# Kernel optimization log

Hardware: AMD Instinct MI355X
Metric: run time of the kernel (lower is better)

The kernel has to match this reference:

```python
import jax, jax.numpy as jnp
import numpy as np

B, S, D, H = 4, 2048, 512, 8
KD = D // H          # key_dim == head_dim == 64
FFN = 4 * D

def _ln(x, g, b, eps):
    mu = x.mean(-1, keepdims=True)
    var = ((x - mu) ** 2).mean(-1, keepdims=True)
    return (x - mu) / jnp.sqrt(var + eps) * g + b

def setup_inputs():
    key = jax.random.key(0)
    ks = jax.random.split(key, 8)
    def lin(k, o, i, scale=0.02):
        k1, k2 = jax.random.split(k)
        return (jax.random.normal(k1, (o, i), jnp.float32) * scale,
                jax.random.normal(k2, (o,), jnp.float32) * scale)
    wq, bq = lin(ks[0], D, D)
    wk, bk = lin(ks[1], D, D)
    wv, bv = lin(ks[2], D, D)
    wg, bg = lin(ks[3], D, D)
    wo, bo = lin(ks[4], D, D)
    fc1_w, fc1_b = lin(ks[5], FFN, D)
    fc2_w, fc2_b = lin(ks[6], D, FFN)
    return {
        'src': jax.random.normal(ks[7], (B, S, D), jnp.float32),
        'mask': jnp.zeros((S, S), jnp.bool_),
        'padding_mask': jnp.zeros((B, S), jnp.bool_),
        'wq': wq, 'bq': bq, 'wk': wk, 'bk': bk, 'wv': wv, 'bv': bv,
        'wg': wg, 'bg': bg, 'wo': wo, 'bo': bo,
        'fc1_w': fc1_w, 'fc1_b': fc1_b, 'fc2_w': fc2_w, 'fc2_b': fc2_b,
        'ln_ffn_g': jnp.ones((FFN,), jnp.float32), 'ln_ffn_b': jnp.zeros((FFN,), jnp.float32),
        'n0_g': jnp.ones((D,), jnp.float32), 'n0_b': jnp.zeros((D,), jnp.float32),
        'n1_g': jnp.ones((D,), jnp.float32), 'n1_b': jnp.zeros((D,), jnp.float32),
    }

def reference(src, mask, padding_mask, wq, bq, wk, bk, wv, bv, wg, bg, wo, bo,
              fc1_w, fc1_b, fc2_w, fc2_b, ln_ffn_g, ln_ffn_b, n0_g, n0_b, n1_g, n1_b):
    b, s, d = src.shape
    # RetNet per-head decay mask (h, s, s): exp((i-j)*log(gamma_h)) on the lower triangle,
    # row-normalized by sqrt(row sum) (torchscale RetNetRelPos, parallel mode).
    idx = jnp.arange(s)
    diff = (idx[:, None] - idx[None, :]).astype(src.dtype)
    decay = jnp.log(1.0 - 2.0 ** (-5.0 - jnp.arange(H, dtype=src.dtype)))
    dm = jnp.where(diff[None] >= 0, jnp.exp(diff[None] * decay[:, None, None]), 0.0)
    dm = dm / jnp.sqrt(dm.sum(-1, keepdims=True))
    # projections; k scaled by key_dim**-0.5 before head split
    q = (src @ wq.T + bq).reshape(b, s, H, KD).transpose(0, 2, 1, 3)
    k = ((src @ wk.T + bk) * (KD ** -0.5)).reshape(b, s, H, KD).transpose(0, 2, 1, 3)
    v = src @ wv.T + bv
    g = src @ wg.T + bg
    # parallel retention: additive decay bias, detached L1 row normalization
    qk = jnp.einsum('bhid,bhjd->bhij', q, k) + dm[None]
    den = jnp.maximum(jnp.abs(jax.lax.stop_gradient(qk).sum(-1, keepdims=True)), 1.0)
    qk = qk / den
    vr = v.reshape(b, s, H, KD).transpose(0, 2, 1, 3)
    o = jnp.einsum('bhij,bhjd->bhid', qk, vr).transpose(0, 2, 1, 3)  # (b,s,h,hd)
    # per-head LayerNorm, eps=1e-6, no affine
    mu = o.mean(-1, keepdims=True)
    o = (o - mu) / jnp.sqrt(((o - mu) ** 2).mean(-1, keepdims=True) + 1e-6)
    o = jax.nn.silu(g) * o.reshape(b, s, d)
    o = o @ wo.T + bo
    # post-norm residual layout
    x = _ln(src + o, n0_g, n0_b, 1e-5)
    h = jax.nn.gelu(x @ fc1_w.T + fc1_b, approximate=False)
    h = _ln(h, ln_ffn_g, ln_ffn_b, 1e-6)  # subln
    h = h @ fc2_w.T + fc2_b
    return _ln(x + h, n1_g, n1_b, 1e-5)
```

## Files before the change

### kernel.cpp

```cpp
#include <hip/hip_runtime.h>
#include <hip/hip_bf16.h>
#include <math.h>

#define DEV __device__ __forceinline__

typedef __attribute__((ext_vector_type(4))) float f32x4;
typedef __attribute__((ext_vector_type(16))) float f32x16;
typedef __attribute__((ext_vector_type(8))) short bf16x8;
typedef __attribute__((ext_vector_type(8))) unsigned short u16x8;
typedef unsigned short u16;
typedef unsigned int u32;
typedef __attribute__((ext_vector_type(4))) u32 u32x4;

DEV u16 f2bf(float f) {
  union { float f; u32 u; } v; v.f = f;
  u32 r = v.u + 0x7fffu + ((v.u >> 16) & 1u);
  return (u16)(r >> 16);
}
DEV float bf2f(u16 h) {
  union { u32 u; float f; } v; v.u = ((u32)h) << 16;
  return v.f;
}

DEV void gl_lds16(const u16* g, u16* s) {
  __builtin_amdgcn_global_load_lds((const __attribute__((address_space(1))) void*)g,
                                   (__attribute__((address_space(3))) void*)s, 16, 0, 0);
}

DEV u32 cvt_pk_bf16(float lo, float hi) {
  u32 r;
  asm("v_cvt_pk_bf16_f32 %0, %1, %2" : "=v"(r) : "v"(lo), "v"(hi));
  return r;
}

DEV bf16x8 u4_to_bf8(u32x4 x) {
  union { u32x4 a; bf16x8 b; } u; u.a = x; return u.b;
}

#define MFMA16(a, b, c) __builtin_amdgcn_mfma_f32_16x16x32_bf16((a), (b), (c), 0, 0, 0)
#define MFMA32(a, b, c) __builtin_amdgcn_mfma_f32_32x32x16_bf16((a), (b), (c), 0, 0, 0)

DEV void cast8(const float* in, u16* out, float s) {
  f32x4 a = *(const f32x4*)in;
  f32x4 b = *(const f32x4*)(in + 4);
  u16x8 r;
  r[0] = f2bf(a[0] * s); r[1] = f2bf(a[1] * s); r[2] = f2bf(a[2] * s); r[3] = f2bf(a[3] * s);
  r[4] = f2bf(b[0] * s); r[5] = f2bf(b[1] * s); r[6] = f2bf(b[2] * s); r[7] = f2bf(b[3] * s);
  *(u16x8*)out = r;
}

__global__ __launch_bounds__(256) void prep_cast(
    const float* __restrict__ src, const float* __restrict__ wq, const float* __restrict__ wk,
    const float* __restrict__ wv, const float* __restrict__ wg, const float* __restrict__ wo,
    const float* __restrict__ fc1, const float* __restrict__ fc2,
    const float* __restrict__ bq, const float* __restrict__ bk,
    const float* __restrict__ bv, const float* __restrict__ bg,
    u16* __restrict__ src_bf, u16* __restrict__ Wcat, u16* __restrict__ wo_bf,
    u16* __restrict__ fc1_bf, u16* __restrict__ fc2_bf, float* __restrict__ bcat) {
  int u = blockIdx.x * 256 + threadIdx.x;
  if (u < 524288) {
    cast8(src + (size_t)u * 8, src_bf + (size_t)u * 8, 1.0f);
  } else if (u < 557056) {
    int v = u - 524288; cast8(wq + (size_t)v * 8, Wcat + (size_t)v * 8, 1.0f);
  } else if (u < 589824) {
    int v = u - 557056; cast8(wk + (size_t)v * 8, Wcat + 262144 + (size_t)v * 8, 0.125f);
  } else if (u < 622592) {
    int v = u - 589824; cast8(wv + (size_t)v * 8, Wcat + 524288 + (size_t)v * 8, 1.0f);
  } else if (u < 655360) {
    int v = u - 622592; cast8(wg + (size_t)v * 8, Wcat + 786432 + (size_t)v * 8, 1.0f);
  } else if (u < 688128) {
    int v = u - 655360; cast8(wo + (size_t)v * 8, wo_bf + (size_t)v * 8, 1.0f);
  } else if (u < 819200) {
    int v = u - 688128; cast8(fc1 + (size_t)v * 8, fc1_bf + (size_t)v * 8, 1.0f);
  } else if (u < 950272) {
    int v = u - 819200; cast8(fc2 + (size_t)v * 8, fc2_bf + (size_t)v * 8, 1.0f);
  } else if (u < 950528) {
    int v = u - 950272;
    #pragma unroll
    for (int e = 0; e < 8; e++) {
      int c = v * 8 + e;
      float val;
      if (c < 512)       val = bq[c];
      else if (c < 1024) val = bk[c - 512] * 0.125f;
      else if (c < 1536) val = bv[c - 1024];
      else               val = bg[c - 1536];
      bcat[c] = val;
    }
  }
}

template <int ACT>
__global__ __launch_bounds__(256) void gemm_v3(
    const u16* __restrict__ A, const u16* __restrict__ W, const float* __restrict__ bias,
    u16* __restrict__ Ob, int N, int K, int TN) {
  __shared__ __align__(16) u16 sm[2][16384];
  const int t = threadIdx.x, l = t & 63;
  const int w = t >> 6, wr = (w >> 1) * 64, wc = (w & 1) * 64;
  const int lc = l & 15, lch = l >> 4;
  const int NT = K >> 6;

  const int orig = blockIdx.x;
  const int cpx = gridDim.x >> 3;
  const int sid = (orig & 7) * cpx + (orig >> 3);
  const int bm = (sid / TN) * 128, bn = (sid % TN) * 128;

  const int srow = t >> 3, sc8 = t & 7;
  const u16* stA = A + (size_t)(bm + srow) * K + ((sc8 ^ (srow & 7)) * 8);
  const u16* stB = W + (size_t)(bn + srow) * K + ((sc8 ^ (srow & 7)) * 8);

#define STAGE(bidx, kt)                                                        \
  {                                                                            \
    u16* d = (u16*)sm[bidx] + t * 8;                                           \
    _Pragma("unroll")                                                          \
    for (int j = 0; j < 4; j++)                                                \
      gl_lds16(stA + (size_t)j * 32 * K + (kt), d + j * 2048);                 \
    _Pragma("unroll")                                                          \
    for (int j = 0; j < 4; j++)                                                \
      gl_lds16(stB + (size_t)j * 32 * K + (kt), d + 8192 + j * 2048);          \
  }

  f32x4 acc[4][4] = {};

  STAGE(0, 0)
  __syncthreads();

  for (int tt = 0; tt < NT; ++tt) {
    if (tt + 1 < NT) STAGE((tt + 1) & 1, (tt + 1) * 64)
    const u16* bufp = sm[tt & 1];
    bf16x8 af[4][2], bfv[4][2];
    #pragma unroll
    for (int mi = 0; mi < 4; mi++) {
      const int row = wr + mi * 16 + lc;
      #pragma unroll
      for (int ks = 0; ks < 2; ks++) {
        const int ch = ks * 4 + lch;
        af[mi][ks] = *(const bf16x8*)&bufp[row * 64 + ((ch ^ (row & 7)) * 8)];
      }
    }
    #pragma unroll
    for (int ni = 0; ni < 4; ni++) {
      const int row = wc + ni * 16 + lc;
      #pragma unroll
      for (int ks = 0; ks < 2; ks++) {
        const int ch = ks * 4 + lch;
        bfv[ni][ks] = *(const bf16x8*)&bufp[8192 + row * 64 + ((ch ^ (row & 7)) * 8)];
      }
    }
    #pragma unroll
    for (int ks = 0; ks < 2; ks++)
      #pragma unroll
      for (int mi = 0; mi < 4; mi++)
        #pragma unroll
        for (int ni = 0; ni < 4; ni++)
          acc[mi][ni] = MFMA16(af[mi][ks], bfv[ni][ks], acc[mi][ni]);
    __syncthreads();
  }
#undef STAGE

  u16* osm = (u16*)sm;
  #pragma unroll
  for (int ni = 0; ni < 4; ni++) {
    const int col = wc + ni * 16 + lc;
    const float bb = bias[bn + col];
    const int ckey = col >> 3, clow = col & 7;
    #pragma unroll
    for (int mi = 0; mi < 4; mi++) {
      #pragma unroll
      for (int r = 0; r < 4; r++) {
        const int row = wr + mi * 16 + lch * 4 + r;
        float v = acc[mi][ni][r] + bb;
        if (ACT == 1) v = 0.5f * v * (1.0f + erff(v * 0.70710678118f));
        osm[row * 128 + ((ckey ^ ((row & 7) << 1)) << 3) + clow] = f2bf(v);
      }
    }
  }
  __syncthreads();
  #pragma unroll
  for (int p = 0; p < 8; p++) {
    const int flat = p * 256 + t;
    const int row = flat >> 4, c = flat & 15;
    u16x8 y = *(const u16x8*)&osm[row * 128 + ((c ^ ((row & 7) << 1)) << 3)];
    *(u16x8*)&Ob[(size_t)(bm + row) * N + bn + c * 8] = y;
  }
}

template <int ACT>
__global__ __launch_bounds__(256) void gemm_m64(
    const u16* __restrict__ A, const u16* __restrict__ W, const float* __restrict__ bias,
    u16* __restrict__ Ob, int N, int K, int TN) {
  __shared__ __align__(16) u16 sm[2][12288];
  const int t = threadIdx.x, l = t & 63;
  const int w = t >> 6, wr = (w >> 1) * 32, wc = (w & 1) * 64;
  const int lc = l & 15, lch = l >> 4;
  const int NT = K >> 6;

  const int orig = blockIdx.x;
  const int cpx = gridDim.x >> 3;
  const int sid = (orig & 7) * cpx + (orig >> 3);
  const int bm = (sid / TN) * 64, bn = (sid % TN) * 128;

  const int srow = t >> 3, sc8 = t & 7;
  const u16* stA = A + (size_t)(bm + srow) * K + ((sc8 ^ (srow & 7)) * 8);
  const u16* stB = W + (size_t)(bn + srow) * K + ((sc8 ^ (srow & 7)) * 8);

#define STAGE(bidx, kt)                                                        \
  {                                                                            \
    u16* d = (u16*)sm[bidx] + t * 8;                                           \
    _Pragma("unroll")                                                          \
    for (int j = 0; j < 2; j++)                                                \
      gl_lds16(stA + (size_t)j * 32 * K + (kt), d + j * 2048);                 \
    _Pragma("unroll")                                                          \
    for (int j = 0; j < 4; j++)                                                \
      gl_lds16(stB + (size_t)j * 32 * K + (kt), d + 4096 + j * 2048);          \
  }

  f32x4 acc[2][4] = {};

  STAGE(0, 0)
  __syncthreads();

  for (int tt = 0; tt < NT; ++tt) {
    if (tt + 1 < NT) STAGE((tt + 1) & 1, (tt + 1) * 64)
    const u16* bufp = sm[tt & 1];
    bf16x8 af[2][2], bfv[4][2];
    #pragma unroll
    for (int mi = 0; mi < 2; mi++) {
      const int row = wr + mi * 16 + lc;
      #pragma unroll
      for (int ks = 0; ks < 2; ks++) {
        const int ch = ks * 4 + lch;
        af[mi][ks] = *(const bf16x8*)&bufp[row * 64 + ((ch ^ (row & 7)) * 8)];
      }
    }
    #pragma unroll
    for (int ni = 0; ni < 4; ni++) {
      const int row = wc + ni * 16 + lc;
      #pragma unroll
      for (int ks = 0; ks < 2; ks++) {
        const int ch = ks * 4 + lch;
        bfv[ni][ks] = *(const bf16x8*)&bufp[4096 + row * 64 + ((ch ^ (row & 7)) * 8)];
      }
    }
    #pragma unroll
    for (int ks = 0; ks < 2; ks++)
      #pragma unroll
      for (int mi = 0; mi < 2; mi++)
        #pragma unroll
        for (int ni = 0; ni < 4; ni++)
          acc[mi][ni] = MFMA16(af[mi][ks], bfv[ni][ks], acc[mi][ni]);
    __syncthreads();
  }
#undef STAGE

  u16* osm = (u16*)sm;
  #pragma unroll
  for (int ni = 0; ni < 4; ni++) {
    const int col = wc + ni * 16 + lc;
    const float bb = bias[bn + col];
    const int ckey = col >> 3, clow = col & 7;
    #pragma unroll
    for (int mi = 0; mi < 2; mi++) {
      #pragma unroll
      for (int r = 0; r < 4; r++) {
        const int row = wr + mi * 16 + lch * 4 + r;
        float v = acc[mi][ni][r] + bb;
        if (ACT == 1) v = 0.5f * v * (1.0f + erff(v * 0.70710678118f));
        osm[row * 128 + ((ckey ^ ((row & 7) << 1)) << 3) + clow] = f2bf(v);
      }
    }
  }
  __syncthreads();
  #pragma unroll
  for (int p = 0; p < 4; p++) {
    const int flat = p * 256 + t;
    const int row = flat >> 4, c = flat & 15;
    u16x8 y = *(const u16x8*)&osm[row * 128 + ((c ^ ((row & 7) << 1)) << 3)];
    *(u16x8*)&Ob[(size_t)(bm + row) * N + bn + c * 8] = y;
  }
}

__global__ __launch_bounds__(256) void vtrans(
    const u16* __restrict__ qkvg, u16* __restrict__ vtg) {
  __shared__ u16 L[64 * 72];
  const int t = threadIdx.x;
  const int jt = blockIdx.x * 64, bh = blockIdx.y, b = bh >> 3, h = bh & 7;
  const u16* src = qkvg + (size_t)(b * 2048 + jt) * 2048 + 1024 + h * 64;
  const int r0 = t >> 3, c0 = (t & 7) * 8;
  u16x8 a0 = *(const u16x8*)(src + (size_t)r0 * 2048 + c0);
  u16x8 a1 = *(const u16x8*)(src + (size_t)(r0 + 32) * 2048 + c0);
  #pragma unroll
  for (int e = 0; e < 8; e++) {
    L[(c0 + e) * 72 + r0] = a0[e];
    L[(c0 + e) * 72 + 32 + r0] = a1[e];
  }
  __syncthreads();
  u16* dst = vtg + (size_t)bh * 64 * 2048 + jt;
  *(u16x8*)(dst + (size_t)r0 * 2048 + c0) = *(const u16x8*)&L[r0 * 72 + c0];
  *(u16x8*)(dst + (size_t)(r0 + 32) * 2048 + c0) = *(const u16x8*)&L[(r0 + 32) * 72 + c0];
}

__global__ __launch_bounds__(512, 4) void retention_v3(
    const u16* __restrict__ qkvg, const u16* __restrict__ vtg, u16* __restrict__ gated) {
  const int S = 2048, DD = 2048;
  const int bh = blockIdx.x, b = bh >> 3, h = bh & 7;
  const int t = threadIdx.x, l = t & 63, w = t >> 6;
  const int lid = l & 31, hi = l >> 5;
  const int g = w >> 2, w4 = w & 3;
  const int wrow = blockIdx.y * 128 + w4 * 32;
  const int i_q = wrow + lid;

  __shared__ __align__(16) u16 sm[32768];

  const size_t base = (size_t)b * S * DD + (size_t)h * 64;
  const u16* qp = qkvg + base;
  const u16* kp = qkvg + base + 512;
  const u16* gp = qkvg + base + 1536;
  const u16* vtp = vtg + (size_t)bh * 64 * S;

  const float l2g = log2f(1.0f - exp2f(-5.0f - (float)h));
  const float rrs = rsqrtf((1.0f - exp2f((float)(i_q + 1) * l2g)) * exp2f(5.0f + (float)h));
  float bjc[16];
  #pragma unroll
  for (int r = 0; r < 16; r++) {
    int joff = (r & 3) + 8 * (r >> 2) + 4 * hi;
    bjc[r] = exp2f(-(float)joff * l2g);
  }

  bf16x8 qf[4];
  #pragma unroll
  for (int ks = 0; ks < 4; ks++)
    qf[ks] = *(const bf16x8*)(qp + (size_t)i_q * DD + ks * 16 + 8 * hi);

  f32x16 accO0, accO1;
  #pragma unroll
  for (int r = 0; r < 16; r++) { accO0[r] = 0.0f; accO1[r] = 0.0f; }
  float den_acc = 0.0f;

  const int srow = t >> 3, sc = t & 7;
  const u16* kg = kp + (size_t)srow * DD + ((sc ^ (srow & 7)) * 8);
  const u16* vg = vtp + (size_t)srow * S + ((sc ^ (srow & 7)) * 8);

#define RSTG(tile)                                                   \
  {                                                                  \
    const int sl_ = (tile) & 3;                                      \
    gl_lds16(kg + (size_t)(tile) * 64 * DD, sm + sl_ * 4096 + t * 8);\
    gl_lds16(vg + (tile) * 64, sm + 16384 + sl_ * 4096 + t * 8);     \
  }

  RSTG(0)
  RSTG(1)
  __syncthreads();

  for (int m = 0; m < 16; ++m) {
    if (m < 15) { RSTG(2 * m + 2) RSTG(2 * m + 3) }
    const int tile = 2 * m + g;
    const int jt = tile * 64;
    const u16* KsB = sm + (tile & 3) * 4096;
    const u16* VtB = sm + 16384 + (tile & 3) * 4096;

    #pragma unroll
    for (int jsub = 0; jsub < 2; jsub++) {
      f32x16 s;
      #pragma unroll
      for (int r = 0; r < 16; r++) s[r] = 0.0f;
      #pragma unroll
      for (int ks = 0; ks < 4; ks++) {
        bf16x8 kf = *(const bf16x8*)&KsB[(jsub * 32 + lid) * 64 +
                                         (((2 * ks + hi) ^ (lid & 7)) * 8)];
        s = MFMA32(kf, qf[ks], s);
      }
      {
        const int js = jt + jsub * 32;
        if (js <= wrow + 31) {
          float bcoef = exp2f((float)(i_q - js) * l2g) * rrs;
          if (js + 31 <= wrow) {
            #pragma unroll
            for (int r = 0; r < 16; r++) s[r] += bcoef * bjc[r];
          } else {
            const int dmax = i_q - js;
            #pragma unroll
            for (int r = 0; r < 16; r++) {
              int joff = (r & 3) + 8 * (r >> 2) + 4 * hi;
              s[r] += (joff <= dmax) ? bcoef * bjc[r] : 0.0f;
            }
          }
        }
      }
      #pragma unroll
      for (int r = 0; r < 16; r++) den_acc += s[r];
      u32 pk[8];
      #pragma unroll
      for (int q = 0; q < 4; q++) {
        pk[q * 2 + 0] = cvt_pk_bf16(s[4 * q + 0], s[4 * q + 1]);
        pk[q * 2 + 1] = cvt_pk_bf16(s[4 * q + 2], s[4 * q + 3]);
      }
      #pragma unroll
      for (int p = 0; p < 2; p++) {
        u32 own0 = hi ? pk[(2 * p + 1) * 2 + 0] : pk[(2 * p) * 2 + 0];
        u32 own1 = hi ? pk[(2 * p + 1) * 2 + 1] : pk[(2 * p) * 2 + 1];
        u32 snd0 = hi ? pk[(2 * p) * 2 + 0] : pk[(2 * p + 1) * 2 + 0];
        u32 snd1 = hi ? pk[(2 * p) * 2 + 1] : pk[(2 * p + 1) * 2 + 1];
        u32 r0 = __shfl_xor(snd0, 32);
        u32 r1 = __shfl_xor(snd1, 32);
        u32x4 paw;
        paw[0] = hi ? r0 : own0;
        paw[1] = hi ? r1 : own1;
        paw[2] = hi ? own0 : r0;
        paw[3] = hi ? own1 : r1;
        bf16x8 paf = u4_to_bf8(paw);
        const int jsl = jsub * 2 + p;
        bf16x8 vt0 = *(const bf16x8*)&VtB[lid * 64 + (((2 * jsl + hi) ^ (lid & 7)) * 8)];
        bf16x8 vt1 = *(const bf16x8*)&VtB[(32 + lid) * 64 + (((2 * jsl + hi) ^ (lid & 7)) * 8)];
        accO0 = MFMA32(vt0, paf, accO0);
        accO1 = MFMA32(vt1, paf, accO1);
      }
    }
    __syncthreads();
  }
#undef RSTG

  float* red = (float*)sm;
  const int ridx = (w4 * 64 + l) * 33;
  if (w >= 4) {
    #pragma unroll
    for (int r = 0; r < 16; r++) { red[ridx + r] = accO0[r]; red[ridx + 16 + r] = accO1[r]; }
    red[ridx + 32] = den_acc;
  }
  __syncthreads();
  if (w >= 4) return;
  #pragma unroll
  for (int r = 0; r < 16; r++) { accO0[r] += red[ridx + r]; accO1[r] += red[ridx + 16 + r]; }
  den_acc += red[ridx + 32];

  float den = den_acc + __shfl_xor(den_acc, 32);
  float rden = 1.0f / fmaxf(fabsf(den), 1.0f);
  float o0[16], o1[16];
  float s1 = 0.0f, s2 = 0.0f;
  #pragma unroll
  for (int r = 0; r < 16; r++) {
    o0[r] = accO0[r] * rden; s1 += o0[r]; s2 += o0[r] * o0[r];
    o1[r] = accO1[r] * rden; s1 += o1[r]; s2 += o1[r] * o1[r];
  }
  s1 += __shfl_xor(s1, 32);
  s2 += __shfl_xor(s2, 32);
  float mu = s1 * (1.0f / 64.0f);
  float var = s2 * (1.0f / 64.0f) - mu * mu;
  float rv = rsqrtf(var + 1e-6f);

  u16* Ot = sm + 16896 + w4 * 2304;
  #pragma unroll
  for (int r = 0; r < 16; r++) {
    int d = (r & 3) + 8 * (r >> 2) + 4 * hi;
    Ot[lid * 72 + d]      = f2bf((o0[r] - mu) * rv);
    Ot[lid * 72 + 32 + d] = f2bf((o1[r] - mu) * rv);
  }
  {
    const int i2 = l >> 1, half = l & 1;
    const int row = wrow + i2;
    #pragma unroll
    for (int c = 0; c < 4; c++) {
      u16x8 y8 = *(const u16x8*)&Ot[i2 * 72 + half * 32 + c * 8];
      u16x8 g8 = *(const u16x8*)(gp + (size_t)row * DD + half * 32 + c * 8);
      u16x8 o8;
      #pragma unroll
      for (int e = 0; e < 8; e++) {
        float gv = bf2f(g8[e]);
        float sg = gv / (1.0f + __expf(-gv));
        o8[e] = f2bf(bf2f(y8[e]) * sg);
      }
      *(u16x8*)&gated[((size_t)(b * S + row)) * 512 + h * 64 + half * 32 + c * 8] = o8;
    }
  }
}

__global__ __launch_bounds__(256) void add_ln512(
    const float* __restrict__ A, const u16* __restrict__ Bv,
    const float* __restrict__ gam, const float* __restrict__ bet, float eps,
    float* __restrict__ Of, u16* __restrict__ Ob) {
  int row = blockIdx.x * 4 + (threadIdx.x >> 6);
  int l = threadIdx.x & 63;
  const float* a = A + (size_t)row * 512 + l * 8;
  f32x4 a0 = *(const f32x4*)a, a1 = *(const f32x4*)(a + 4);
  u16x8 cv = *(const u16x8*)(Bv + (size_t)row * 512 + l * 8);
  float x[8];
  #pragma unroll
  for (int e = 0; e < 4; e++) { x[e] = a0[e] + bf2f(cv[e]); x[4 + e] = a1[e] + bf2f(cv[4 + e]); }
  float s = 0.f, s2 = 0.f;
  #pragma unroll
  for (int e = 0; e < 8; e++) { s += x[e]; s2 += x[e] * x[e]; }
  #pragma unroll
  for (int m = 1; m <= 32; m <<= 1) { s += __shfl_xor(s, m); s2 += __shfl_xor(s2, m); }
  float mu = s * (1.0f / 512.0f);
  float var = s2 * (1.0f / 512.0f) - mu * mu;
  float rinv = rsqrtf(var + eps);
  f32x4 g0 = *(const f32x4*)(gam + l * 8), g1 = *(const f32x4*)(gam + l * 8 + 4);
  f32x4 b0 = *(const f32x4*)(bet + l * 8), b1 = *(const f32x4*)(bet + l * 8 + 4);
  f32x4 y0, y1;
  #pragma unroll
  for (int e = 0; e < 4; e++) {
    y0[e] = (x[e] - mu) * rinv * g0[e] + b0[e];
    y1[e] = (x[4 + e] - mu) * rinv * g1[e] + b1[e];
  }
  float* op = Of + (size_t)row * 512 + l * 8;
  *(f32x4*)op = y0;
  *(f32x4*)(op + 4) = y1;
  if (Ob) {
    u16x8 rb_;
    #pragma unroll
    for (int e = 0; e < 4; e++) { rb_[e] = f2bf(y0[e]); rb_[4 + e] = f2bf(y1[e]); }
    *(u16x8*)(Ob + (size_t)row * 512 + l * 8) = rb_;
  }
}

__global__ __launch_bounds__(256) void subln_ffn(
    u16* __restrict__ hbuf, const float* __restrict__ gam, const float* __restrict__ bet) {
  int row = blockIdx.x * 4 + (threadIdx.x >> 6);
  int l = threadIdx.x & 63;
  u16* p = hbuf + (size_t)row * 2048;
  float x[32];
  #pragma unroll
  for (int cch = 0; cch < 4; cch++) {
    u16x8 v = *(const u16x8*)(p + cch * 512 + l * 8);
    #pragma unroll
    for (int e = 0; e < 8; e++) x[cch * 8 + e] = bf2f(v[e]);
  }
  float s = 0.f, s2 = 0.f;
  #pragma unroll
  for (int e = 0; e < 32; e++) { s += x[e]; s2 += x[e] * x[e]; }
  #pragma unroll
  for (int m = 1; m <= 32; m <<= 1) { s += __shfl_xor(s, m); s2 += __shfl_xor(s2, m); }
  float mu = s * (1.0f / 2048.0f);
  float var = s2 * (1.0f / 2048.0f) - mu * mu;
  float rinv = rsqrtf(var + 1e-6f);
  #pragma unroll
  for (int cch = 0; cch < 4; cch++) {
    int col = cch * 512 + l * 8;
    f32x4 g0 = *(const f32x4*)(gam + col), g1 = *(const f32x4*)(gam + col + 4);
    f32x4 b0 = *(const f32x4*)(bet + col), b1 = *(const f32x4*)(bet + col + 4);
    u16x8 o;
    #pragma unroll
    for (int e = 0; e < 4; e++) {
      o[e]     = f2bf((x[cch * 8 + e]     - mu) * rinv * g0[e] + b0[e]);
      o[4 + e] = f2bf((x[cch * 8 + 4 + e] - mu) * rinv * g1[e] + b1[e]);
    }
    *(u16x8*)(p + col) = o;
  }
}

extern "C" void kernel_launch(void* const* d_in, const int* in_sizes, int n_in,
                              void* d_out, int out_size, void* d_ws, size_t ws_size,
                              hipStream_t stream) {
  const float* src  = (const float*)d_in[0];
  const float* wq   = (const float*)d_in[3];
  const float* bq   = (const float*)d_in[4];
  const float* wk   = (const float*)d_in[5];
  const float* bk   = (const float*)d_in[6];
  const float* wv   = (const float*)d_in[7];
  const float* bv   = (const float*)d_in[8];
  const float* wg   = (const float*)d_in[9];
  const float* bg   = (const float*)d_in[10];
  const float* wo   = (const float*)d_in[11];
  const float* bo   = (const float*)d_in[12];
  const float* fc1w = (const float*)d_in[13];
  const float* fc1b = (const float*)d_in[14];
  const float* fc2w = (const float*)d_in[15];
  const float* fc2b = (const float*)d_in[16];
  const float* lng  = (const float*)d_in[17];
  const float* lnb  = (const float*)d_in[18];
  const float* n0g  = (const float*)d_in[19];
  const float* n0b  = (const float*)d_in[20];
  const float* n1g  = (const float*)d_in[21];
  const float* n1b  = (const float*)d_in[22];

  if (ws_size < 90710016u) return;

  char* ws = (char*)d_ws;
  u16*   src_bf = (u16*)(ws + 0);
  u16*   Wcat   = (u16*)(ws + 8388608);
  u16*   wo_bf  = (u16*)(ws + 10485760);
  u16*   fc1_bf = (u16*)(ws + 11010048);
  u16*   fc2_bf = (u16*)(ws + 13107200);
  float* bcat   = (float*)(ws + 15204352);
  u16*   qkvg   = (u16*)(ws + 15212544);
  u16*   gated  = (u16*)(ws + 48766976);
  u16*   attn   = (u16*)(ws + 57155584);
  float* xf     = (float*)(ws + 65544192);
  u16*   xbf    = (u16*)(ws + 82321408);
  u16*   vtg    = (u16*)(ws + 65544192);

  prep_cast<<<3713, 256, 0, stream>>>(src, wq, wk, wv, wg, wo, fc1w, fc2w,
                                      bq, bk, bv, bg,
                                      src_bf, Wcat, wo_bf, fc1_bf, fc2_bf, bcat);
  gemm_v3<0><<<1024, 256, 0, stream>>>(src_bf, Wcat, bcat, qkvg, 2048, 512, 16);
  vtrans<<<dim3(32, 32), 256, 0, stream>>>(qkvg, vtg);
  retention_v3<<<dim3(32, 16), 512, 0, stream>>>(qkvg, vtg, gated);
  gemm_m64<0><<<512, 256, 0, stream>>>(gated, wo_bf, bo, attn, 512, 512, 4);
  add_ln512<<<2048, 256, 0, stream>>>(src, attn, n0g, n0b, 1e-5f, xf, xbf);
  gemm_v3<1><<<1024, 256, 0, stream>>>(xbf, fc1_bf, fc1b, qkvg, 2048, 512, 16);
  subln_ffn<<<2048, 256, 0, stream>>>(qkvg, lng, lnb);
  gemm_m64<0><<<512, 256, 0, stream>>>(qkvg, fc2_bf, fc2b, attn, 512, 2048, 4);
  add_ln512<<<2048, 256, 0, stream>>>(xf, attn, n1g, n1b, 1e-5f, (float*)d_out, nullptr);
}
```

Baseline: 205.2 us.

## Give each retention wave its own query rows instead of splitting keys across wave groups

The retention kernel now assigns all 8 waves distinct 32-row query blocks (256 rows per workgroup) and has every wave stream all 32 key tiles, instead of two wave groups each covering half the key tiles and then reducing through LDS. Key and value staging becomes a double buffer with explicit vmcnt waits and raw barriers, and s_setprio is raised around the MFMA sections. This removes the cross-group LDS reduction and halves the LDS footprint. In exchange the grid is halved to 256 workgroups, so fewer workgroups are available to fill the CUs.

Measured after the change: 188.3 us. -8.2%, faster.

```diff
diff --git a/kernel.cpp b/kernel.cpp
--- a/kernel.cpp
+++ b/kernel.cpp
@@ -35,6 +35,14 @@
 
 DEV bf16x8 u4_to_bf8(u32x4 x) {
   union { u32x4 a; bf16x8 b; } u; u.a = x; return u.b;
+}
+
+DEV void barrier_() {
+  __builtin_amdgcn_sched_barrier(0);
+  asm volatile("" ::: "memory");
+  __builtin_amdgcn_s_barrier();
+  asm volatile("" ::: "memory");
+  __builtin_amdgcn_sched_barrier(0);
 }
 
 #define MFMA16(a, b, c) __builtin_amdgcn_mfma_f32_16x16x32_bf16((a), (b), (c), 0, 0, 0)
@@ -299,17 +307,16 @@
   *(u16x8*)(dst + (size_t)(r0 + 32) * 2048 + c0) = *(const u16x8*)&L[(r0 + 32) * 72 + c0];
 }
 
-__global__ __launch_bounds__(512, 4) void retention_v3(
+__global__ __launch_bounds__(512) void retention_v4(
     const u16* __restrict__ qkvg, const u16* __restrict__ vtg, u16* __restrict__ gated) {
   const int S = 2048, DD = 2048;
   const int bh = blockIdx.x, b = bh >> 3, h = bh & 7;
   const int t = threadIdx.x, l = t & 63, w = t >> 6;
   const int lid = l & 31, hi = l >> 5;
-  const int g = w >> 2, w4 = w & 3;
-  const int wrow = blockIdx.y * 128 + w4 * 32;
+  const int wrow = blockIdx.y * 256 + w * 32;
   const int i_q = wrow + lid;
 
-  __shared__ __align__(16) u16 sm[32768];
+  __shared__ __align__(16) u16 sm[18432];
 
   const size_t base = (size_t)b * S * DD + (size_t)h * 64;
   const u16* qp = qkvg + base;
@@ -340,35 +347,41 @@
   const u16* kg = kp + (size_t)srow * DD + ((sc ^ (srow & 7)) * 8);
   const u16* vg = vtp + (size_t)srow * S + ((sc ^ (srow & 7)) * 8);
 
-#define RSTG(tile)                                                   \
-  {                                                                  \
-    const int sl_ = (tile) & 3;                                      \
-    gl_lds16(kg + (size_t)(tile) * 64 * DD, sm + sl_ * 4096 + t * 8);\
-    gl_lds16(vg + (tile) * 64, sm + 16384 + sl_ * 4096 + t * 8);     \
+#define RSTG(tile)                                                    \
+  {                                                                   \
+    const int sl_ = (tile) & 1;                                       \
+    gl_lds16(kg + (size_t)(tile) * 64 * DD, sm + sl_ * 4096 + t * 8); \
+    gl_lds16(vg + (tile) * 64, sm + 8192 + sl_ * 4096 + t * 8);       \
   }
 
   RSTG(0)
-  RSTG(1)
-  __syncthreads();
-
-  for (int m = 0; m < 16; ++m) {
-    if (m < 15) { RSTG(2 * m + 2) RSTG(2 * m + 3) }
-    const int tile = 2 * m + g;
-    const int jt = tile * 64;
-    const u16* KsB = sm + (tile & 3) * 4096;
-    const u16* VtB = sm + 16384 + (tile & 3) * 4096;
+
+  for (int m = 0; m < 32; ++m) {
+    if (m < 31) {
+      RSTG(m + 1)
+      asm volatile("s_waitcnt vmcnt(2)" ::: "memory");
+    } else {
+      asm volatile("s_waitcnt vmcnt(0)" ::: "memory");
+    }
+    barrier_();
+
+    const int jt = m * 64;
+    const u16* KsB = sm + (m & 1) * 4096;
+    const u16* VtB = sm + 8192 + (m & 1) * 4096;
 
     #pragma unroll
     for (int jsub = 0; jsub < 2; jsub++) {
       f32x16 s;
       #pragma unroll
       for (int r = 0; r < 16; r++) s[r] = 0.0f;
+      __builtin_amdgcn_s_setprio(1);
       #pragma unroll
       for (int ks = 0; ks < 4; ks++) {
         bf16x8 kf = *(const bf16x8*)&KsB[(jsub * 32 + lid) * 64 +
                                          (((2 * ks + hi) ^ (lid & 7)) * 8)];
         s = MFMA32(kf, qf[ks], s);
       }
+      __builtin_amdgcn_s_setprio(0);
       {
         const int js = jt + jsub * 32;
         if (js <= wrow + 31) {
@@ -411,26 +424,16 @@
         const int jsl = jsub * 2 + p;
         bf16x8 vt0 = *(const bf16x8*)&VtB[lid * 64 + (((2 * jsl + hi) ^ (lid & 7)) * 8)];
         bf16x8 vt1 = *(const bf16x8*)&VtB[(32 + lid) * 64 + (((2 * jsl + hi) ^ (lid & 7)) * 8)];
+        __builtin_amdgcn_s_setprio(1);
         accO0 = MFMA32(vt0, paf, accO0);
         accO1 = MFMA32(vt1, paf, accO1);
-      }
-    }
-    __syncthreads();
+        __builtin_amdgcn_s_setprio(0);
+      }
+    }
+    asm volatile("s_waitcnt lgkmcnt(0)" ::: "memory");
+    barrier_();
   }
 #undef RSTG
-
-  float* red = (float*)sm;
-  const int ridx = (w4 * 64 + l) * 33;
-  if (w >= 4) {
-    #pragma unroll
-    for (int r = 0; r < 16; r++) { red[ridx + r] = accO0[r]; red[ridx + 16 + r] = accO1[r]; }
-    red[ridx + 32] = den_acc;
-  }
-  __syncthreads();
-  if (w >= 4) return;
-  #pragma unroll
-  for (int r = 0; r < 16; r++) { accO0[r] += red[ridx + r]; accO1[r] += red[ridx + 16 + r]; }
-  den_acc += red[ridx + 32];
 
   float den = den_acc + __shfl_xor(den_acc, 32);
   float rden = 1.0f / fmaxf(fabsf(den), 1.0f);
@@ -447,7 +450,7 @@
   float var = s2 * (1.0f / 64.0f) - mu * mu;
   float rv = rsqrtf(var + 1e-6f);
 
-  u16* Ot = sm + 16896 + w4 * 2304;
+  u16* Ot = sm + w * 2304;
   #pragma unroll
   for (int r = 0; r < 16; r++) {
     int d = (r & 3) + 8 * (r >> 2) + 4 * hi;
@@ -593,7 +596,7 @@
                                       src_bf, Wcat, wo_bf, fc1_bf, fc2_bf, bcat);
   gemm_v3<0><<<1024, 256, 0, stream>>>(src_bf, Wcat, bcat, qkvg, 2048, 512, 16);
   vtrans<<<dim3(32, 32), 256, 0, stream>>>(qkvg, vtg);
-  retention_v3<<<dim3(32, 16), 512, 0, stream>>>(qkvg, vtg, gated);
+  retention_v4<<<dim3(32, 8), 512, 0, stream>>>(qkvg, vtg, gated);
   gemm_m64<0><<<512, 256, 0, stream>>>(gated, wo_bf, bo, attn, 512, 512, 4);
   add_ln512<<<2048, 256, 0, stream>>>(src, attn, n0g, n0b, 1e-5f, xf, xbf);
   gemm_v3<1><<<1024, 256, 0, stream>>>(xbf, fc1_bf, fc1b, qkvg, 2048, 512, 16);
```

## Replace quadratic retention with linear-attention form plus chunked decay scan

Applied to the files above, without the earlier changes.

The decay bias in this task is added to the scores, not multiplied, and the q·k scores carry no causal mask. So the output splits into q·(KᵀV) over the whole sequence plus a decayed causal sum of V. The change computes KᵀV per head once, and builds the decayed V sum with a per-chunk kernel and a sequential scan across chunks. The denominator is computed in closed form as q·sum(k) plus the square root of the row sum. This removes the O(S²) score and PV MFMA work and its K/V streaming, at the cost of several small extra launches (transpose, scan, KᵀV), a low-parallelism scan with only 32 blocks, and storing KᵀV in bf16.

Measured after the change: 185.6 us. 1.11x faster.

```diff
diff --git a/kernel.cpp b/kernel.cpp
--- a/kernel.cpp
+++ b/kernel.cpp
@@ -10,7 +10,6 @@
 typedef __attribute__((ext_vector_type(8))) unsigned short u16x8;
 typedef unsigned short u16;
 typedef unsigned int u32;
-typedef __attribute__((ext_vector_type(4))) u32 u32x4;
 
 DEV u16 f2bf(float f) {
   union { float f; u32 u; } v; v.f = f;
@@ -21,20 +20,13 @@
   union { u32 u; float f; } v; v.u = ((u32)h) << 16;
   return v.f;
 }
+DEV float bfel(bf16x8 v, int e) {
+  union { bf16x8 b; u16x8 u; } x; x.b = v; return bf2f(x.u[e]);
+}
 
 DEV void gl_lds16(const u16* g, u16* s) {
   __builtin_amdgcn_global_load_lds((const __attribute__((address_space(1))) void*)g,
                                    (__attribute__((address_space(3))) void*)s, 16, 0, 0);
-}
-
-DEV u32 cvt_pk_bf16(float lo, float hi) {
-  u32 r;
-  asm("v_cvt_pk_bf16_f32 %0, %1, %2" : "=v"(r) : "v"(lo), "v"(hi));
-  return r;
-}
-
-DEV bf16x8 u4_to_bf8(u32x4 x) {
-  union { u32x4 a; bf16x8 b; } u; u.a = x; return u.b;
 }
 
 #define MFMA16(a, b, c) __builtin_amdgcn_mfma_f32_16x16x32_bf16((a), (b), (c), 0, 0, 0)
@@ -279,161 +271,215 @@
   }
 }
 
-__global__ __launch_bounds__(256) void vtrans(
-    const u16* __restrict__ qkvg, u16* __restrict__ vtg) {
-  __shared__ u16 L[64 * 72];
+__global__ __launch_bounds__(256) void transkv(
+    const u16* __restrict__ qkvg, u16* __restrict__ ktg, u16* __restrict__ vtg,
+    float* __restrict__ Wtab) {
+  __shared__ u16 Lk[64 * 72], Lv[64 * 72];
   const int t = threadIdx.x;
-  const int jt = blockIdx.x * 64, bh = blockIdx.y, b = bh >> 3, h = bh & 7;
-  const u16* src = qkvg + (size_t)(b * 2048 + jt) * 2048 + 1024 + h * 64;
+  const int bh = blockIdx.x, c = blockIdx.y, b = bh >> 3, h = bh & 7;
+  const int jt = c * 64;
+  const u16* kptr = qkvg + (size_t)(b * 2048 + jt) * 2048 + 512 + h * 64;
+  const u16* vptr = kptr + 512;
   const int r0 = t >> 3, c0 = (t & 7) * 8;
-  u16x8 a0 = *(const u16x8*)(src + (size_t)r0 * 2048 + c0);
-  u16x8 a1 = *(const u16x8*)(src + (size_t)(r0 + 32) * 2048 + c0);
+  u16x8 k0 = *(const u16x8*)(kptr + (size_t)r0 * 2048 + c0);
+  u16x8 k1 = *(const u16x8*)(kptr + (size_t)(r0 + 32) * 2048 + c0);
+  u16x8 v0 = *(const u16x8*)(vptr + (size_t)r0 * 2048 + c0);
+  u16x8 v1 = *(const u16x8*)(vptr + (size_t)(r0 + 32) * 2048 + c0);
   #pragma unroll
   for (int e = 0; e < 8; e++) {
-    L[(c0 + e) * 72 + r0] = a0[e];
-    L[(c0 + e) * 72 + 32 + r0] = a1[e];
-  }
-  __syncthreads();
-  u16* dst = vtg + (size_t)bh * 64 * 2048 + jt;
-  *(u16x8*)(dst + (size_t)r0 * 2048 + c0) = *(const u16x8*)&L[r0 * 72 + c0];
-  *(u16x8*)(dst + (size_t)(r0 + 32) * 2048 + c0) = *(const u16x8*)&L[(r0 + 32) * 72 + c0];
-}
-
-__global__ __launch_bounds__(512, 4) void retention_v3(
-    const u16* __restrict__ qkvg, const u16* __restrict__ vtg, u16* __restrict__ gated) {
+    Lk[(c0 + e) * 72 + r0] = k0[e];  Lk[(c0 + e) * 72 + 32 + r0] = k1[e];
+    Lv[(c0 + e) * 72 + r0] = v0[e];  Lv[(c0 + e) * 72 + 32 + r0] = v1[e];
+  }
+  __syncthreads();
+  {
+    u16* kd = ktg + (size_t)bh * 64 * 2048 + jt;
+    u16* vd = vtg + (size_t)bh * 64 * 2048 + jt;
+    *(u16x8*)(kd + (size_t)r0 * 2048 + c0)        = *(const u16x8*)&Lk[r0 * 72 + c0];
+    *(u16x8*)(kd + (size_t)(r0 + 32) * 2048 + c0) = *(const u16x8*)&Lk[(r0 + 32) * 72 + c0];
+    *(u16x8*)(vd + (size_t)r0 * 2048 + c0)        = *(const u16x8*)&Lv[r0 * 72 + c0];
+    *(u16x8*)(vd + (size_t)(r0 + 32) * 2048 + c0) = *(const u16x8*)&Lv[(r0 + 32) * 72 + c0];
+  }
+  if (t < 64) {
+    const float gamma = 1.0f - exp2f(-5.0f - (float)h);
+    float acc = 0.0f, p = 1.0f;
+    for (int jj = 0; jj < 64; jj++) {
+      acc += p * bf2f(Lv[t * 72 + (63 - jj)]);
+      p *= gamma;
+    }
+    Wtab[((size_t)bh * 32 + c) * 64 + t] = acc;
+  }
+}
+
+__global__ __launch_bounds__(256) void scan_kernel(
+    const u16* __restrict__ ktg, float* __restrict__ Ctab, float* __restrict__ ksum) {
+  __shared__ float ps[4][64];
+  const int t = threadIdx.x, bh = blockIdx.x, h = bh & 7;
+  const int a = t & 63, q = t >> 6;
+  const u16* kr = ktg + (size_t)bh * 64 * 2048 + (size_t)a * 2048 + q * 512;
+  float s = 0.0f;
+  for (int j = 0; j < 512; j += 8) {
+    u16x8 v = *(const u16x8*)(kr + j);
+    #pragma unroll
+    for (int e = 0; e < 8; e++) s += bf2f(v[e]);
+  }
+  ps[q][a] = s;
+  __syncthreads();
+  if (t < 64) {
+    ksum[bh * 64 + t] = ps[0][t] + ps[1][t] + ps[2][t] + ps[3][t];
+    const float gamma = 1.0f - exp2f(-5.0f - (float)h);
+    const float g64 = exp2f(64.0f * log2f(gamma));
+    float* Wp = Ctab + (size_t)bh * 32 * 64 + t;
+    float C = 0.0f;
+    for (int c = 0; c < 32; c++) {
+      C = C * g64 + Wp[c * 64];
+      Wp[c * 64] = C;
+    }
+  }
+}
+
+__global__ __launch_bounds__(256) void vtk_kernel(
+    const u16* __restrict__ vtg, const u16* __restrict__ ktg, u16* __restrict__ vtk) {
+  __shared__ float red[3][4096];
+  const int t = threadIdx.x, l = t & 63, w = t >> 6;
+  const int bh = blockIdx.x;
+  const int lc = l & 15, lch = l >> 4;
+  const u16* vb = vtg + (size_t)bh * 64 * 2048;
+  const u16* kb = ktg + (size_t)bh * 64 * 2048;
+  f32x4 acc[4][4] = {};
+  for (int it = 0; it < 16; ++it) {
+    const int j0 = w * 512 + it * 32 + lch * 8;
+    bf16x8 af[4], bfr[4];
+    #pragma unroll
+    for (int mt = 0; mt < 4; mt++)
+      af[mt] = *(const bf16x8*)(vb + (size_t)(mt * 16 + lc) * 2048 + j0);
+    #pragma unroll
+    for (int nt = 0; nt < 4; nt++)
+      bfr[nt] = *(const bf16x8*)(kb + (size_t)(nt * 16 + lc) * 2048 + j0);
+    #pragma unroll
+    for (int mt = 0; mt < 4; mt++)
+      #pragma unroll
+      for (int nt = 0; nt < 4; nt++)
+        acc[mt][nt] = MFMA16(af[mt], bfr[nt], acc[mt][nt]);
+  }
+  if (w > 0) {
+    #pragma unroll
+    for (int mt = 0; mt < 4; mt++)
+      #pragma unroll
+      for (int nt = 0; nt < 4; nt++)
+        #pragma unroll
+        for (int r = 0; r < 4; r++)
+          red[w - 1][(mt * 16 + lch * 4 + r) * 64 + nt * 16 + lc] = acc[mt][nt][r];
+  }
+  __syncthreads();
+  if (w == 0) {
+    u16* out = vtk + (size_t)bh * 64 * 64;
+    #pragma unroll
+    for (int mt = 0; mt < 4; mt++)
+      #pragma unroll
+      for (int nt = 0; nt < 4; nt++)
+        #pragma unroll
+        for (int r = 0; r < 4; r++) {
+          int row = mt * 16 + lch * 4 + r, col = nt * 16 + lc;
+          float v = acc[mt][nt][r] + red[0][row * 64 + col] + red[1][row * 64 + col] +
+                    red[2][row * 64 + col];
+          out[row * 64 + col] = f2bf(v);
+        }
+  }
+}
+
+__global__ __launch_bounds__(512) void ret_out(
+    const u16* __restrict__ qkvg, const u16* __restrict__ vtg,
+    const u16* __restrict__ vtk, const float* __restrict__ Ctab,
+    const float* __restrict__ ksum, u16* __restrict__ gated) {
   const int S = 2048, DD = 2048;
   const int bh = blockIdx.x, b = bh >> 3, h = bh & 7;
   const int t = threadIdx.x, l = t & 63, w = t >> 6;
   const int lid = l & 31, hi = l >> 5;
-  const int g = w >> 2, w4 = w & 3;
-  const int wrow = blockIdx.y * 128 + w4 * 32;
+  const int wrow = blockIdx.y * 256 + w * 32;
   const int i_q = wrow + lid;
-
-  __shared__ __align__(16) u16 sm[32768];
+  const int chunk = wrow >> 6;
+  const int iloc = i_q & 63;
+
+  __shared__ __align__(16) u16 sm[18432];
+  float* smf = (float*)sm;
 
   const size_t base = (size_t)b * S * DD + (size_t)h * 64;
   const u16* qp = qkvg + base;
-  const u16* kp = qkvg + base + 512;
   const u16* gp = qkvg + base + 1536;
-  const u16* vtp = vtg + (size_t)bh * 64 * S;
-
-  const float l2g = log2f(1.0f - exp2f(-5.0f - (float)h));
-  const float rrs = rsqrtf((1.0f - exp2f((float)(i_q + 1) * l2g)) * exp2f(5.0f + (float)h));
-  float bjc[16];
-  #pragma unroll
-  for (int r = 0; r < 16; r++) {
-    int joff = (r & 3) + 8 * (r >> 2) + 4 * hi;
-    bjc[r] = exp2f(-(float)joff * l2g);
-  }
+
+  const float gamma = 1.0f - exp2f(-5.0f - (float)h);
+  const float l2g = log2f(gamma);
+  const float rowsum = (1.0f - exp2f((float)(i_q + 1) * l2g)) * exp2f(5.0f + (float)h);
+  const float rrs = rsqrtf(rowsum);
+
+  {
+    const int il = t >> 3, j0 = (t & 7) * 8;
+    u16x8 row;
+    #pragma unroll
+    for (int e = 0; e < 8; e++) {
+      int d = il - (j0 + e);
+      row[e] = (d >= 0) ? f2bf(exp2f((float)d * l2g)) : (u16)0;
+    }
+    *(u16x8*)&sm[il * 72 + j0] = row;
+  }
+  if (t < 256) {
+    int cc = blockIdx.y * 4 - 1 + (t >> 6);
+    smf[4608 + t] = (cc >= 0) ? Ctab[((size_t)bh * 32 + cc) * 64 + (t & 63)] : 0.0f;
+  } else if (t < 320) {
+    smf[4864 + (t - 256)] = ksum[bh * 64 + (t - 256)];
+  }
+  __syncthreads();
 
   bf16x8 qf[4];
   #pragma unroll
-  for (int ks = 0; ks < 4; ks++)
-    qf[ks] = *(const bf16x8*)(qp + (size_t)i_q * DD + ks * 16 + 8 * hi);
+  for (int kc = 0; kc < 4; kc++)
+    qf[kc] = *(const bf16x8*)(qp + (size_t)i_q * DD + kc * 16 + 8 * hi);
+
+  const u16* vt_b = vtg + (size_t)bh * 64 * S;
+  const u16* vk_b = vtk + (size_t)bh * 64 * 64;
 
   f32x16 accO0, accO1;
   #pragma unroll
   for (int r = 0; r < 16; r++) { accO0[r] = 0.0f; accO1[r] = 0.0f; }
-  float den_acc = 0.0f;
-
-  const int srow = t >> 3, sc = t & 7;
-  const u16* kg = kp + (size_t)srow * DD + ((sc ^ (srow & 7)) * 8);
-  const u16* vg = vtp + (size_t)srow * S + ((sc ^ (srow & 7)) * 8);
-
-#define RSTG(tile)                                                   \
-  {                                                                  \
-    const int sl_ = (tile) & 3;                                      \
-    gl_lds16(kg + (size_t)(tile) * 64 * DD, sm + sl_ * 4096 + t * 8);\
-    gl_lds16(vg + (tile) * 64, sm + 16384 + sl_ * 4096 + t * 8);     \
-  }
-
-  RSTG(0)
-  RSTG(1)
-  __syncthreads();
-
-  for (int m = 0; m < 16; ++m) {
-    if (m < 15) { RSTG(2 * m + 2) RSTG(2 * m + 3) }
-    const int tile = 2 * m + g;
-    const int jt = tile * 64;
-    const u16* KsB = sm + (tile & 3) * 4096;
-    const u16* VtB = sm + 16384 + (tile & 3) * 4096;
-
-    #pragma unroll
-    for (int jsub = 0; jsub < 2; jsub++) {
-      f32x16 s;
-      #pragma unroll
-      for (int r = 0; r < 16; r++) s[r] = 0.0f;
-      #pragma unroll
-      for (int ks = 0; ks < 4; ks++) {
-        bf16x8 kf = *(const bf16x8*)&KsB[(jsub * 32 + lid) * 64 +
-                                         (((2 * ks + hi) ^ (lid & 7)) * 8)];
-        s = MFMA32(kf, qf[ks], s);
-      }
-      {
-        const int js = jt + jsub * 32;
-        if (js <= wrow + 31) {
-          float bcoef = exp2f((float)(i_q - js) * l2g) * rrs;
-          if (js + 31 <= wrow) {
-            #pragma unroll
-            for (int r = 0; r < 16; r++) s[r] += bcoef * bjc[r];
-          } else {
-            const int dmax = i_q - js;
-            #pragma unroll
-            for (int r = 0; r < 16; r++) {
-              int joff = (r & 3) + 8 * (r >> 2) + 4 * hi;
-              s[r] += (joff <= dmax) ? bcoef * bjc[r] : 0.0f;
-            }
-          }
-        }
-      }
-      #pragma unroll
-      for (int r = 0; r < 16; r++) den_acc += s[r];
-      u32 pk[8];
-      #pragma unroll
-      for (int q = 0; q < 4; q++) {
-        pk[q * 2 + 0] = cvt_pk_bf16(s[4 * q + 0], s[4 * q + 1]);
-        pk[q * 2 + 1] = cvt_pk_bf16(s[4 * q + 2], s[4 * q + 3]);
-      }
-      #pragma unroll
-      for (int p = 0; p < 2; p++) {
-        u32 own0 = hi ? pk[(2 * p + 1) * 2 + 0] : pk[(2 * p) * 2 + 0];
-        u32 own1 = hi ? pk[(2 * p + 1) * 2 + 1] : pk[(2 * p) * 2 + 1];
-        u32 snd0 = hi ? pk[(2 * p) * 2 + 0] : pk[(2 * p + 1) * 2 + 0];
-        u32 snd1 = hi ? pk[(2 * p) * 2 + 1] : pk[(2 * p + 1) * 2 + 1];
-        u32 r0 = __shfl_xor(snd0, 32);
-        u32 r1 = __shfl_xor(snd1, 32);
-        u32x4 paw;
-        paw[0] = hi ? r0 : own0;
-        paw[1] = hi ? r1 : own1;
-        paw[2] = hi ? own0 : r0;
-        paw[3] = hi ? own1 : r1;
-        bf16x8 paf = u4_to_bf8(paw);
-        const int jsl = jsub * 2 + p;
-        bf16x8 vt0 = *(const bf16x8*)&VtB[lid * 64 + (((2 * jsl + hi) ^ (lid & 7)) * 8)];
-        bf16x8 vt1 = *(const bf16x8*)&VtB[(32 + lid) * 64 + (((2 * jsl + hi) ^ (lid & 7)) * 8)];
-        accO0 = MFMA32(vt0, paf, accO0);
-        accO1 = MFMA32(vt1, paf, accO1);
-      }
-    }
-    __syncthreads();
-  }
-#undef RSTG
-
-  float* red = (float*)sm;
-  const int ridx = (w4 * 64 + l) * 33;
-  if (w >= 4) {
-    #pragma unroll
-    for (int r = 0; r < 16; r++) { red[ridx + r] = accO0[r]; red[ridx + 16 + r] = accO1[r]; }
-    red[ridx + 32] = den_acc;
-  }
-  __syncthreads();
-  if (w >= 4) return;
-  #pragma unroll
-  for (int r = 0; r < 16; r++) { accO0[r] += red[ridx + r]; accO1[r] += red[ridx + 16 + r]; }
-  den_acc += red[ridx + 32];
-
-  float den = den_acc + __shfl_xor(den_acc, 32);
+
+  #pragma unroll
+  for (int kc = 0; kc < 4; kc++) {
+    bf16x8 lb = *(const bf16x8*)&sm[iloc * 72 + kc * 16 + hi * 8];
+    bf16x8 va0 = *(const bf16x8*)(vt_b + (size_t)lid * S + chunk * 64 + kc * 16 + hi * 8);
+    bf16x8 va1 = *(const bf16x8*)(vt_b + (size_t)(lid + 32) * S + chunk * 64 + kc * 16 + hi * 8);
+    accO0 = MFMA32(va0, lb, accO0);
+    accO1 = MFMA32(va1, lb, accO1);
+  }
+  {
+    const float gpw = exp2f((float)(iloc + 1) * l2g);
+    const float* Cst = &smf[4608 + (w >> 1) * 64];
+    #pragma unroll
+    for (int r = 0; r < 16; r++) {
+      int br = (r & 3) + 8 * (r >> 2) + 4 * hi;
+      accO0[r] += gpw * Cst[br];
+      accO1[r] += gpw * Cst[32 + br];
+    }
+  }
+  #pragma unroll
+  for (int r = 0; r < 16; r++) { accO0[r] *= rrs; accO1[r] *= rrs; }
+  #pragma unroll
+  for (int kc = 0; kc < 4; kc++) {
+    bf16x8 ka0 = *(const bf16x8*)(vk_b + (size_t)lid * 64 + kc * 16 + hi * 8);
+    bf16x8 ka1 = *(const bf16x8*)(vk_b + (size_t)(lid + 32) * 64 + kc * 16 + hi * 8);
+    accO0 = MFMA32(ka0, qf[kc], accO0);
+    accO1 = MFMA32(ka1, qf[kc], accO1);
+  }
+  float dsum = 0.0f;
+  #pragma unroll
+  for (int kc = 0; kc < 4; kc++) {
+    const float* Ks = &smf[4864 + kc * 16 + hi * 8];
+    #pragma unroll
+    for (int e = 0; e < 8; e++) dsum += bfel(qf[kc], e) * Ks[e];
+  }
+  dsum += __shfl_xor(dsum, 32);
+  float den = dsum + sqrtf(rowsum);
   float rden = 1.0f / fmaxf(fabsf(den), 1.0f);
+
   float o0[16], o1[16];
   float s1 = 0.0f, s2 = 0.0f;
   #pragma unroll
@@ -447,7 +493,9 @@
   float var = s2 * (1.0f / 64.0f) - mu * mu;
   float rv = rsqrtf(var + 1e-6f);
 
-  u16* Ot = sm + 16896 + w4 * 2304;
+  __syncthreads();
+
+  u16* Ot = sm + w * 2304;
   #pragma unroll
   for (int r = 0; r < 16; r++) {
     int d = (r & 3) + 8 * (r >> 2) + 4 * hi;
@@ -572,7 +620,7 @@
   const float* n1g  = (const float*)d_in[21];
   const float* n1b  = (const float*)d_in[22];
 
-  if (ws_size < 90710016u) return;
+  if (ws_size < 91242496u) return;
 
   char* ws = (char*)d_ws;
   u16*   src_bf = (u16*)(ws + 0);
@@ -585,15 +633,21 @@
   u16*   gated  = (u16*)(ws + 48766976);
   u16*   attn   = (u16*)(ws + 57155584);
   float* xf     = (float*)(ws + 65544192);
+  u16*   vtg    = (u16*)(ws + 65544192);
+  u16*   ktg    = (u16*)(ws + 73932800);
   u16*   xbf    = (u16*)(ws + 82321408);
-  u16*   vtg    = (u16*)(ws + 65544192);
+  float* Ctab   = (float*)(ws + 90710016);
+  u16*   vtkb   = (u16*)(ws + 90972160);
+  float* ksumb  = (float*)(ws + 91234304);
 
   prep_cast<<<3713, 256, 0, stream>>>(src, wq, wk, wv, wg, wo, fc1w, fc2w,
                                       bq, bk, bv, bg,
                                       src_bf, Wcat, wo_bf, fc1_bf, fc2_bf, bcat);
   gemm_v3<0><<<1024, 256, 0, stream>>>(src_bf, Wcat, bcat, qkvg, 2048, 512, 16);
-  vtrans<<<dim3(32, 32), 256, 0, stream>>>(qkvg, vtg);
-  retention_v3<<<dim3(32, 16), 512, 0, stream>>>(qkvg, vtg, gated);
+  transkv<<<dim3(32, 32), 256, 0, stream>>>(qkvg, ktg, vtg, Ctab);
+  scan_kernel<<<32, 256, 0, stream>>>(ktg, Ctab, ksumb);
+  vtk_kernel<<<32, 256, 0, stream>>>(vtg, ktg, vtkb);
+  ret_out<<<dim3(32, 8), 512, 0, stream>>>(qkvg, vtg, vtkb, Ctab, ksumb, gated);
   gemm_m64<0><<<512, 256, 0, stream>>>(gated, wo_bf, bo, attn, 512, 512, 4);
   add_ln512<<<2048, 256, 0, stream>>>(src, attn, n0g, n0b, 1e-5f, xf, xbf);
   gemm_v3<1><<<1024, 256, 0, stream>>>(xbf, fc1_bf, fc1b, qkvg, 2048, 512, 16);
```
